# Kernel optimization log

Measured on AMD Instinct MI355X. Metric: run time of the kernel, lower is better.

## Reference

```python
import jax, jax.numpy as jnp
import numpy as np

MASK_VALUE = -10000000.0


def setup_inputs() -> dict:
    key = jax.random.key(0)
    ks = jax.random.split(key, 8)
    U, I, J, C, E = 128, 256, 512, 128, 128
    return {
        "target_items_context": jax.random.normal(ks[0], (U, I, C), jnp.float32),
        "interacted_items_context": jax.random.normal(ks[1], (U, J, C), jnp.float32),
        "user_embeds": jax.random.normal(ks[2], (U, E), jnp.float32),
        "attention_mask": jax.random.randint(ks[3], (U, J), 0, 2) > 0,
        "w_dense": jax.random.normal(ks[4], (2 * C,), jnp.float32) * 0.02,
        "b_dense": jax.random.normal(ks[5], (1,), jnp.float32) * 0.02,
        "W_mlp": jax.random.normal(ks[6], (E + C, C), jnp.float32) * 0.02,
        "b_mlp": jax.random.normal(ks[7], (C,), jnp.float32) * 0.02,
    }


def reference(target_items_context, interacted_items_context, user_embeds,
              attention_mask, w_dense, b_dense, W_mlp, b_mlp):
    C = target_items_context.shape[-1]
    E = user_embeds.shape[-1]
    # additive attention score: tanh([t; k] @ w + b) = tanh(t@w1 + k@w2 + b)
    # (dropout is identity in eval mode)
    s_t = jnp.einsum('uic,c->ui', target_items_context, w_dense[:C])      # (U, I)
    s_k = jnp.einsum('ujc,c->uj', interacted_items_context, w_dense[C:])  # (U, J)
    scores = jnp.tanh(s_t[:, :, None] + s_k[:, None, :] + b_dense[0])     # (U, I, J)
    scores = scores + (~attention_mask)[:, None, :].astype(scores.dtype) * MASK_VALUE
    attn = jax.nn.softmax(scores, axis=-1)                                # (U, I, J)
    # weighted pooling of interacted contexts
    pooled = jnp.einsum('uij,ujc->uic', attn, interacted_items_context)   # (U, I, C)
    # mlp: relu([user; pooled] @ W + b) = relu(user@W[:E] + pooled@W[E:] + b)
    u_part = user_embeds @ W_mlp[:E]                                      # (U, C)
    user_context = jax.nn.relu(u_part[:, None, :] + pooled @ W_mlp[E:] + b_mlp)
    return user_context, attn
```

## Files before the change

### kernel.cpp

```cpp
#include <hip/hip_runtime.h>

#define UU 128
#define II 256
#define JJ 512
#define CC 128
#define EE 128
#define IB2 32
#define NIB2 8
#define JT 64
#define NJT 8
#define VTP 72
#define IBF 16

typedef short bf16x8 __attribute__((ext_vector_type(8)));
typedef float f32x4 __attribute__((ext_vector_type(4)));

union FragU { bf16x8 v; unsigned u[4]; };

__device__ __forceinline__ float fast_tanh(float x) {
    float ex = __expf(2.0f * x);
    return 1.0f - 2.0f / (ex + 1.0f);
}

__device__ __forceinline__ unsigned pack_bf16x2(float lo, float hi) {
    unsigned ul = __float_as_uint(lo), uh = __float_as_uint(hi);
    ul = (ul + 0x7FFFu + ((ul >> 16) & 1u)) >> 16;
    uh = (uh + 0x7FFFu + ((uh >> 16) & 1u)) >> 16;
    return ul | (uh << 16);
}

__device__ __forceinline__ short bf16s(float f) {
    unsigned u = __float_as_uint(f);
    u = (u + 0x7FFFu + ((u >> 16) & 1u)) >> 16;
    return (short)u;
}

__device__ __forceinline__ float wave_reduce_add(float v) {
#pragma unroll
    for (int k = 32; k >= 1; k >>= 1) v += __shfl_xor(v, k, 64);
    return v;
}

#define VT_BLOCKS (UU * NJT)
#define UP_BLOCKS (UU * CC / 256)

__global__ void precompute_kernel(const float* __restrict__ itc,
                                  const float* __restrict__ user,
                                  const float* __restrict__ wd,
                                  const float* __restrict__ Wm,
                                  const float* __restrict__ bm,
                                  float* __restrict__ sk_g,
                                  float* __restrict__ up_g,
                                  short* __restrict__ vtg,
                                  short* __restrict__ wtg) {
    __shared__ float vt_f[JT][CC + 4];
    int b = blockIdx.x;
    int t = threadIdx.x;
    if (b < VT_BLOCKS) {
        int u = b & 127, jt = b >> 7;
        const float* src = itc + ((size_t)u * JJ + jt * JT) * CC;
#pragma unroll
        for (int k = 0; k < 8; ++k) {
            int f = t + 256 * k;
            int row = f >> 5, c4 = (f & 31) * 4;
            f32x4 v = __builtin_nontemporal_load(
                (const f32x4*)&src[(size_t)row * CC + c4]);
            *(f32x4*)&vt_f[row][c4] = v;
        }
        __syncthreads();
        {
            int r = t >> 2, q4 = t & 3;
            float s = 0.f;
#pragma unroll
            for (int cc = 0; cc < 32; cc += 4) {
                float4 a = *(const float4*)&vt_f[r][q4 * 32 + cc];
                float4 w = *(const float4*)&wd[CC + q4 * 32 + cc];
                s += a.x * w.x + a.y * w.y + a.z * w.z + a.w * w.w;
            }
            s += __shfl_xor(s, 1, 64);
            s += __shfl_xor(s, 2, 64);
            if (q4 == 0) sk_g[u * JJ + jt * JT + r] = s;
        }
        {
            int c = t & 127, half = t >> 7;
            unsigned* dst = (unsigned*)(vtg + (size_t)(u * NJT + jt) * 8192) +
                            half * 2048 + c * 16;
#pragma unroll
            for (int m4 = 0; m4 < 4; ++m4) {
                unsigned q[4];
#pragma unroll
                for (int mm = 0; mm < 4; ++mm) {
                    int m = 4 * m4 + mm;
                    q[mm] = pack_bf16x2(vt_f[32 * half + 2 * m][c],
                                        vt_f[32 * half + 2 * m + 1][c]);
                }
                *(uint4*)&dst[4 * m4] = make_uint4(q[0], q[1], q[2], q[3]);
            }
        }
    } else if (b < VT_BLOCKS + UP_BLOCKS) {
        int idx = (b - VT_BLOCKS) * 256 + t;
        int u = idx >> 7, c = idx & 127;
        float acc = bm[c];
#pragma unroll 8
        for (int e = 0; e < EE; ++e) acc += user[u * EE + e] * Wm[e * CC + c];
        up_g[idx] = acc;
    } else {
        int n = t & 127, khalf = t >> 7;
#pragma unroll
        for (int ks2 = 0; ks2 < 2; ++ks2) {
            int ks = khalf * 2 + ks2;
#pragma unroll
            for (int g = 0; g < 4; ++g) {
                unsigned q[4];
#pragma unroll
                for (int pr = 0; pr < 4; ++pr) {
                    float lo = Wm[(size_t)(EE + 32 * ks + 8 * g + 2 * pr) * CC + n];
                    float hi = Wm[(size_t)(EE + 32 * ks + 8 * g + 2 * pr + 1) * CC + n];
                    q[pr] = pack_bf16x2(lo, hi);
                }
                *(uint4*)&wtg[ks * 4096 + n * 32 + 8 * g] =
                    make_uint4(q[0], q[1], q[2], q[3]);
            }
        }
    }
}

__global__ __launch_bounds__(256, 4) void fused_main(
    const float* __restrict__ tgt, const int* __restrict__ mask,
    const float* __restrict__ wd, const float* __restrict__ bd,
    const float* __restrict__ sk_g, const float* __restrict__ up_g,
    const short* __restrict__ vt_g, const short* __restrict__ wt_g,
    float* __restrict__ out_ctx, float* __restrict__ out_attn) {
    __shared__ __align__(16) short ps[16384];
    __shared__ float dinv_lds[IB2];

    int b = blockIdx.x;
    int x = b & 7, q = b >> 3;
    int u = x + 8 * (q >> 3);
    int ib = q & 7;
    int i0 = ib * IB2;
    int t = threadIdx.x;
    int w = t >> 6, l = t & 63, ln = l & 15, g = l >> 4;
    int r2 = t >> 3, seg8 = t & 7;
    int tile = r2 >> 4, rr = r2 & 15;

    float sv;
    {
        const float* trow = tgt + ((size_t)(u * II + i0 + r2)) * CC + seg8 * 16;
        f32x4 t0 = __builtin_nontemporal_load((const f32x4*)&trow[0]);
        f32x4 t1 = __builtin_nontemporal_load((const f32x4*)&trow[4]);
        f32x4 t2 = __builtin_nontemporal_load((const f32x4*)&trow[8]);
        f32x4 t3 = __builtin_nontemporal_load((const f32x4*)&trow[12]);
        float4 w0 = *(const float4*)&wd[seg8 * 16];
        float4 w1 = *(const float4*)&wd[seg8 * 16 + 4];
        float4 w2 = *(const float4*)&wd[seg8 * 16 + 8];
        float4 w3 = *(const float4*)&wd[seg8 * 16 + 12];
        float part = t0[0] * w0.x + t0[1] * w0.y + t0[2] * w0.z + t0[3] * w0.w +
                     t1[0] * w1.x + t1[1] * w1.y + t1[2] * w1.z + t1[3] * w1.w +
                     t2[0] * w2.x + t2[1] * w2.y + t2[2] * w2.z + t2[3] * w2.w +
                     t3[0] * w3.x + t3[1] * w3.y + t3[2] * w3.z + t3[3] * w3.w;
        part += __shfl_xor(part, 1, 64);
        part += __shfl_xor(part, 2, 64);
        part += __shfl_xor(part, 4, 64);
        sv = part + bd[0];
    }

    const float* skb = sk_g + u * JJ;
    const int* mkb = mask + u * JJ;
    char* psrow = (char*)ps + tile * 16384 + rr * 1024;
    float rowsum = 0.f;
#pragma unroll 4
    for (int h = 0; h < 8; ++h) {
        int gcol = seg8 + 8 * h;
        int jb = gcol * 8;
        float4 k0 = *(const float4*)&skb[jb];
        float4 k1 = *(const float4*)&skb[jb + 4];
        int4 m0 = *(const int4*)&mkb[jb];
        int4 m1 = *(const int4*)&mkb[jb + 4];
        float p0 = m0.x ? __expf(fast_tanh(sv + k0.x)) : 0.f;
        float p1 = m0.y ? __expf(fast_tanh(sv + k0.y)) : 0.f;
        float p2 = m0.z ? __expf(fast_tanh(sv + k0.z)) : 0.f;
        float p3 = m0.w ? __expf(fast_tanh(sv + k0.w)) : 0.f;
        float p4 = m1.x ? __expf(fast_tanh(sv + k1.x)) : 0.f;
        float p5 = m1.y ? __expf(fast_tanh(sv + k1.y)) : 0.f;
        float p6 = m1.z ? __expf(fast_tanh(sv + k1.z)) : 0.f;
        float p7 = m1.w ? __expf(fast_tanh(sv + k1.w)) : 0.f;
        rowsum += p0 + p1 + p2 + p3 + p4 + p5 + p6 + p7;
        unsigned q0 = pack_bf16x2(p0, p1);
        unsigned q1 = pack_bf16x2(p2, p3);
        unsigned q2 = pack_bf16x2(p4, p5);
        unsigned q3 = pack_bf16x2(p6, p7);
        int gp = gcol ^ (rr & 7);
        *(uint4*)(psrow + 16 * gp) = make_uint4(q0, q1, q2, q3);
    }
    rowsum += __shfl_xor(rowsum, 1, 64);
    rowsum += __shfl_xor(rowsum, 2, 64);
    rowsum += __shfl_xor(rowsum, 4, 64);
    if (seg8 == 0) dinv_lds[r2] = 1.0f / rowsum;

    const short* b_base =
        vt_g + (size_t)u * (NJT * 8192) + (32 * w + ln) * 32 + 8 * g;
    bf16x8 pb0[4], pb1[4];
#pragma unroll
    for (int s = 0; s < 4; ++s) {
        int off = (s >> 1) * 8192 + (s & 1) * 4096;
        pb0[s] = *(const bf16x8*)&b_base[off];
        pb1[s] = *(const bf16x8*)&b_base[off + 512];
    }

    asm volatile("s_waitcnt lgkmcnt(0)" ::: "memory");
    __builtin_amdgcn_s_barrier();
    asm volatile("" ::: "memory");

    f32x4 a00 = {0.f, 0.f, 0.f, 0.f}, a01 = {0.f, 0.f, 0.f, 0.f};
    f32x4 a10 = {0.f, 0.f, 0.f, 0.f}, a11 = {0.f, 0.f, 0.f, 0.f};
    __builtin_amdgcn_s_setprio(1);
#pragma unroll
    for (int s = 0; s < 16; ++s) {
        int abyte = ln * 1024 + 16 * ((4 * s + g) ^ (ln & 7));
        bf16x8 af0 = *(const bf16x8*)((const char*)ps + abyte);
        bf16x8 af1 = *(const bf16x8*)((const char*)ps + 16384 + abyte);
        a00 = __builtin_amdgcn_mfma_f32_16x16x32_bf16(af0, pb0[s & 3], a00, 0, 0, 0);
        a01 = __builtin_amdgcn_mfma_f32_16x16x32_bf16(af0, pb1[s & 3], a01, 0, 0, 0);
        a10 = __builtin_amdgcn_mfma_f32_16x16x32_bf16(af1, pb0[s & 3], a10, 0, 0, 0);
        a11 = __builtin_amdgcn_mfma_f32_16x16x32_bf16(af1, pb1[s & 3], a11, 0, 0, 0);
        if (s < 12) {
            int off = ((s + 4) >> 1) * 8192 + ((s + 4) & 1) * 4096;
            pb0[s & 3] = *(const bf16x8*)&b_base[off];
            pb1[s & 3] = *(const bf16x8*)&b_base[off + 512];
        }
    }
    __builtin_amdgcn_s_setprio(0);

    const short* wbase = wt_g + (32 * w + ln) * 32 + 8 * g;
    bf16x8 wb0[4], wb1[4];
#pragma unroll
    for (int ks = 0; ks < 4; ++ks) {
        wb0[ks] = *(const bf16x8*)&wbase[ks * 4096];
        wb1[ks] = *(const bf16x8*)&wbase[ks * 4096 + 512];
    }
    int c0 = 32 * w + ln, c1 = c0 + 16;
    float up0v = up_g[u * CC + c0];
    float up1v = up_g[u * CC + c1];

    {
        float* ab = out_attn + ((size_t)(u * II + i0)) * JJ;
#pragma unroll
        for (int k = 0; k < 16; ++k) {
            int f = t + 256 * k;
            int row = f >> 7;
            int j4 = (f & 127) * 4;
            int gcol = j4 >> 3, half = (j4 >> 2) & 1;
            int tl = row >> 4, rw = row & 15;
            uint2 qv = *(const uint2*)((const char*)ps + tl * 16384 + rw * 1024 +
                                       16 * (gcol ^ (rw & 7)) + 8 * half);
            float dv = dinv_lds[row];
            f32x4 v;
            v[0] = __uint_as_float(qv.x << 16) * dv;
            v[1] = __uint_as_float(qv.x & 0xFFFF0000u) * dv;
            v[2] = __uint_as_float(qv.y << 16) * dv;
            v[3] = __uint_as_float(qv.y & 0xFFFF0000u) * dv;
            __builtin_nontemporal_store(v, (f32x4*)&ab[(size_t)row * JJ + j4]);
        }
    }

    asm volatile("s_waitcnt lgkmcnt(0)" ::: "memory");
    __builtin_amdgcn_s_barrier();
    asm volatile("" ::: "memory");

    {
        char* pool = (char*)ps;
#pragma unroll
        for (int ri = 0; ri < 4; ++ri) {
            int row0 = 4 * g + ri, row1 = 16 + row0;
            float dv0 = dinv_lds[row0], dv1 = dinv_lds[row1];
            *(short*)(pool + row0 * 256 + 16 * ((c0 >> 3) ^ (row0 & 7)) +
                      2 * (ln & 7)) = bf16s(a00[ri] * dv0);
            *(short*)(pool + row0 * 256 + 16 * ((c1 >> 3) ^ (row0 & 7)) +
                      2 * (ln & 7)) = bf16s(a01[ri] * dv0);
            *(short*)(pool + row1 * 256 + 16 * ((c0 >> 3) ^ (row1 & 7)) +
                      2 * (ln & 7)) = bf16s(a10[ri] * dv1);
            *(short*)(pool + row1 * 256 + 16 * ((c1 >> 3) ^ (row1 & 7)) +
                      2 * (ln & 7)) = bf16s(a11[ri] * dv1);
        }
    }
    asm volatile("s_waitcnt lgkmcnt(0)" ::: "memory");
    __builtin_amdgcn_s_barrier();
    asm volatile("" ::: "memory");

    f32x4 o00 = {0.f, 0.f, 0.f, 0.f}, o01 = {0.f, 0.f, 0.f, 0.f};
    f32x4 o10 = {0.f, 0.f, 0.f, 0.f}, o11 = {0.f, 0.f, 0.f, 0.f};
#pragma unroll
    for (int ks = 0; ks < 4; ++ks) {
        int pbyte0 = ln * 256 + 16 * ((4 * ks + g) ^ (ln & 7));
        bf16x8 pa0 = *(const bf16x8*)((const char*)ps + pbyte0);
        bf16x8 pa1 = *(const bf16x8*)((const char*)ps + 4096 + pbyte0);
        o00 = __builtin_amdgcn_mfma_f32_16x16x32_bf16(pa0, wb0[ks], o00, 0, 0, 0);
        o01 = __builtin_amdgcn_mfma_f32_16x16x32_bf16(pa0, wb1[ks], o01, 0, 0, 0);
        o10 = __builtin_amdgcn_mfma_f32_16x16x32_bf16(pa1, wb0[ks], o10, 0, 0, 0);
        o11 = __builtin_amdgcn_mfma_f32_16x16x32_bf16(pa1, wb1[ks], o11, 0, 0, 0);
    }
    {
        float* ctx = out_ctx + ((size_t)(u * II + i0)) * CC;
#pragma unroll
        for (int ri = 0; ri < 4; ++ri) {
            int row0 = 4 * g + ri, row1 = 16 + row0;
            __builtin_nontemporal_store(fmaxf(o00[ri] + up0v, 0.f),
                                        &ctx[(size_t)row0 * CC + c0]);
            __builtin_nontemporal_store(fmaxf(o01[ri] + up1v, 0.f),
                                        &ctx[(size_t)row0 * CC + c1]);
            __builtin_nontemporal_store(fmaxf(o10[ri] + up0v, 0.f),
                                        &ctx[(size_t)row1 * CC + c0]);
            __builtin_nontemporal_store(fmaxf(o11[ri] + up1v, 0.f),
                                        &ctx[(size_t)row1 * CC + c1]);
        }
    }
}

__global__ __launch_bounds__(256, 3) void fused_fallback(
    const float* __restrict__ tgt, const float* __restrict__ itc,
    const float* __restrict__ user, const int* __restrict__ mask,
    const float* __restrict__ wd, const float* __restrict__ bd,
    const float* __restrict__ Wm, const float* __restrict__ bm,
    float* __restrict__ out_ctx, float* __restrict__ out_attn) {
    __shared__ __align__(16) short Vt[CC][VTP];
    __shared__ __align__(16) float pool[IBF][CC + 4];
    __shared__ __align__(16) float skv[JJ];
    __shared__ __align__(16) float stv[IBF];
    __shared__ __align__(16) float upv[CC];
    __shared__ __align__(16) float dinv_lds[IBF];
    __shared__ unsigned char mk[JJ];

    int b = blockIdx.x;
    int x = b & 7, q = b >> 3;
    int u = x + 8 * (q >> 4);
    int ib = q & 15;
    int i0 = ib * IBF;
    int t = threadIdx.x;

    mk[t] = (unsigned char)(mask[u * JJ + t] != 0);
    mk[t + 256] = (unsigned char)(mask[u * JJ + t + 256] != 0);

    {
        int lane = t & 63, w4 = t >> 6;
        float2 w2 = *(const float2*)&wd[CC + lane * 2];
        for (int r = w4; r < JJ; r += 4) {
            float2 a = *(const float2*)&itc[((size_t)u * JJ + r) * CC + lane * 2];
            float s = wave_reduce_add(a.x * w2.x + a.y * w2.y);
            if (lane == 0) skv[r] = s;
        }
        float2 w1 = *(const float2*)&wd[lane * 2];
        float bdv = bd[0];
        for (int r = w4; r < IBF; r += 4) {
            float2 a = *(const float2*)&tgt[((size_t)u * II + i0 + r) * CC + lane * 2];
            float s = wave_reduce_add(a.x * w1.x + a.y * w1.y);
            if (lane == 0) stv[r] = s + bdv;
        }
        if (t < CC) {
            float acc = bm[t];
            for (int e = 0; e < EE; ++e) acc += user[u * EE + e] * Wm[e * CC + t];
            upv[t] = acc;
        }
    }
    __syncthreads();

    const int l = t & 63;
    const int w = t >> 6;
    const int ln = l & 15;
    const int g = l >> 4;

    bf16x8 a[16];
    float rowsum = 0.0f;
    {
        float s = stv[ln];
#pragma unroll
        for (int t16 = 0; t16 < 16; ++t16) {
            int j = 32 * t16 + 8 * g;
            float4 k0 = *(const float4*)&skv[j];
            float4 k1 = *(const float4*)&skv[j + 4];
            unsigned m0 = *(const unsigned*)&mk[j];
            unsigned m1 = *(const unsigned*)&mk[j + 4];
            float pf[8];
            pf[0] = (m0 & 0x000000FFu) ? __expf(fast_tanh(s + k0.x)) : 0.0f;
            pf[1] = (m0 & 0x0000FF00u) ? __expf(fast_tanh(s + k0.y)) : 0.0f;
            pf[2] = (m0 & 0x00FF0000u) ? __expf(fast_tanh(s + k0.z)) : 0.0f;
            pf[3] = (m0 & 0xFF000000u) ? __expf(fast_tanh(s + k0.w)) : 0.0f;
            pf[4] = (m1 & 0x000000FFu) ? __expf(fast_tanh(s + k1.x)) : 0.0f;
            pf[5] = (m1 & 0x0000FF00u) ? __expf(fast_tanh(s + k1.y)) : 0.0f;
            pf[6] = (m1 & 0x00FF0000u) ? __expf(fast_tanh(s + k1.z)) : 0.0f;
            pf[7] = (m1 & 0xFF000000u) ? __expf(fast_tanh(s + k1.w)) : 0.0f;
            rowsum += pf[0] + pf[1] + pf[2] + pf[3] + pf[4] + pf[5] + pf[6] + pf[7];
            FragU cu;
            cu.u[0] = pack_bf16x2(pf[0], pf[1]);
            cu.u[1] = pack_bf16x2(pf[2], pf[3]);
            cu.u[2] = pack_bf16x2(pf[4], pf[5]);
            cu.u[3] = pack_bf16x2(pf[6], pf[7]);
            a[t16] = cu.v;
        }
    }
    rowsum += __shfl_xor(rowsum, 16, 64);
    rowsum += __shfl_xor(rowsum, 32, 64);
    float dinv = 1.0f / rowsum;
    if (t < 16) dinv_lds[t] = dinv;

    {
        float* abase = out_attn + ((size_t)(u * II + i0 + ln)) * JJ + 8 * g;
#pragma unroll
        for (int t16 = 0; t16 < 16; ++t16) {
            FragU cu; cu.v = a[t16];
            float f0 = __uint_as_float(cu.u[0] << 16) * dinv;
            float f1 = __uint_as_float(cu.u[0] & 0xFFFF0000u) * dinv;
            float f2 = __uint_as_float(cu.u[1] << 16) * dinv;
            float f3 = __uint_as_float(cu.u[1] & 0xFFFF0000u) * dinv;
            float f4 = __uint_as_float(cu.u[2] << 16) * dinv;
            float f5 = __uint_as_float(cu.u[2] & 0xFFFF0000u) * dinv;
            float f6 = __uint_as_float(cu.u[3] << 16) * dinv;
            float f7 = __uint_as_float(cu.u[3] & 0xFFFF0000u) * dinv;
            *(float4*)&abase[32 * t16] = make_float4(f0, f1, f2, f3);
            *(float4*)&abase[32 * t16 + 4] = make_float4(f4, f5, f6, f7);
        }
    }

    f32x4 acc0 = {0.f, 0.f, 0.f, 0.f};
    f32x4 acc1 = {0.f, 0.f, 0.f, 0.f};
    const float* Vu = itc + (size_t)u * JJ * CC;
    const int cg = t & 31;
    const int jp = t >> 5;
    const int n0 = w * 32;

    for (int jt = 0; jt < 8; ++jt) {
        int j0 = jt * JT;
        __syncthreads();
#pragma unroll
        for (int it = 0; it < 4; ++it) {
            int jl = 2 * (jp + 8 * it);
            const float* r0 = &Vu[(size_t)(j0 + jl) * CC];
            const float* r1 = r0 + CC;
#pragma unroll
            for (int qv = 0; qv < 4; ++qv) {
                int c = cg + 32 * qv;
                *(unsigned*)&Vt[c][jl] = pack_bf16x2(r0[c], r1[c]);
            }
        }
        __syncthreads();
#pragma unroll
        for (int kk = 0; kk < 2; ++kk) {
            bf16x8 b0 = *(const bf16x8*)&Vt[n0 + ln][32 * kk + 8 * g];
            bf16x8 b1 = *(const bf16x8*)&Vt[n0 + 16 + ln][32 * kk + 8 * g];
            acc0 = __builtin_amdgcn_mfma_f32_16x16x32_bf16(a[2 * jt + kk], b0,
                                                           acc0, 0, 0, 0);
            acc1 = __builtin_amdgcn_mfma_f32_16x16x32_bf16(a[2 * jt + kk], b1,
                                                           acc1, 0, 0, 0);
        }
    }

    __syncthreads();
    {
        float4 dv = *(const float4*)&dinv_lds[4 * g];
        float dvr[4] = {dv.x, dv.y, dv.z, dv.w};
#pragma unroll
        for (int r = 0; r < 4; ++r) {
            pool[4 * g + r][n0 + ln] = acc0[r] * dvr[r];
            pool[4 * g + r][n0 + 16 + ln] = acc1[r] * dvr[r];
        }
    }
    __syncthreads();

    {
        int tx = t & 15, ty = t >> 4;
        float o[8];
#pragma unroll
        for (int k = 0; k < 8; ++k) o[k] = 0.f;
#pragma unroll 4
        for (int k = 0; k < CC; ++k) {
            float pk = pool[ty][k];
            float4 w0 = *(const float4*)&Wm[(size_t)(EE + k) * CC + tx * 8];
            float4 w1 = *(const float4*)&Wm[(size_t)(EE + k) * CC + tx * 8 + 4];
            o[0] += pk * w0.x; o[1] += pk * w0.y; o[2] += pk * w0.z; o[3] += pk * w0.w;
            o[4] += pk * w1.x; o[5] += pk * w1.y; o[6] += pk * w1.z; o[7] += pk * w1.w;
        }
        float4 up0 = *(const float4*)&upv[tx * 8];
        float4 up1 = *(const float4*)&upv[tx * 8 + 4];
        float4 r0, r1;
        r0.x = fmaxf(o[0] + up0.x, 0.f); r0.y = fmaxf(o[1] + up0.y, 0.f);
        r0.z = fmaxf(o[2] + up0.z, 0.f); r0.w = fmaxf(o[3] + up0.w, 0.f);
        r1.x = fmaxf(o[4] + up1.x, 0.f); r1.y = fmaxf(o[5] + up1.y, 0.f);
        r1.z = fmaxf(o[6] + up1.z, 0.f); r1.w = fmaxf(o[7] + up1.w, 0.f);
        float* ctx = out_ctx + ((size_t)(u * II + i0 + ty)) * CC + tx * 8;
        *(float4*)&ctx[0] = r0;
        *(float4*)&ctx[4] = r1;
    }
}

extern "C" void kernel_launch(void* const* d_in, const int* in_sizes, int n_in,
                              void* d_out, int out_size, void* d_ws,
                              size_t ws_size, hipStream_t stream) {
    const float* tgt  = (const float*)d_in[0];
    const float* itc  = (const float*)d_in[1];
    const float* user = (const float*)d_in[2];
    const int*   mask = (const int*)d_in[3];
    const float* wd   = (const float*)d_in[4];
    const float* bd   = (const float*)d_in[5];
    const float* Wm   = (const float*)d_in[6];
    const float* bm   = (const float*)d_in[7];
    float* out_ctx  = (float*)d_out;
    float* out_attn = out_ctx + (size_t)UU * II * CC;

    size_t scalars = (size_t)(UU * JJ + UU * CC) * sizeof(float);
    size_t vt_bytes = (size_t)UU * NJT * 8192 * sizeof(short);
    size_t wt_bytes = (size_t)16384 * sizeof(short);
    size_t need = scalars + vt_bytes + wt_bytes;
    if (ws_size >= need) {
        float* sk_g = (float*)d_ws;
        float* up_g = sk_g + UU * JJ;
        short* vt_g = (short*)((char*)d_ws + scalars);
        short* wt_g = vt_g + (size_t)UU * NJT * 8192;
        int gridA = VT_BLOCKS + UP_BLOCKS + 1;
        precompute_kernel<<<gridA, 256, 0, stream>>>(itc, user, wd, Wm, bm,
                                                     sk_g, up_g, vt_g, wt_g);
        fused_main<<<UU * NIB2, 256, 0, stream>>>(tgt, mask, wd, bd, sk_g, up_g,
                                                  vt_g, wt_g, out_ctx, out_attn);
    } else {
        fused_fallback<<<UU * (II / IBF), 256, 0, stream>>>(
            tgt, itc, user, mask, wd, bd, Wm, bm, out_ctx, out_attn);
    }
}
```

Baseline: 50.50 us.

## Specialize warps: two waves do the P@V MFMA while two stream the attention output

Work between the four waves is now split by role. Waves 0-1 each compute 64 output columns of the attention-weighted pooling with MFMA, double-buffering their V fragments. Waves 2-3 write the normalized attention matrix to global memory, which lets the global store traffic overlap with the matrix-core work. The cost is that MFMA throughput is concentrated in half the waves and register pressure rises in those waves (eight accumulators).

```diff
diff --git a/kernel.cpp b/kernel.cpp
--- a/kernel.cpp
+++ b/kernel.cpp
@@ -198,69 +198,85 @@
     rowsum += __shfl_xor(rowsum, 4, 64);
     if (seg8 == 0) dinv_lds[r2] = 1.0f / rowsum;
 
-    const short* b_base =
-        vt_g + (size_t)u * (NJT * 8192) + (32 * w + ln) * 32 + 8 * g;
-    bf16x8 pb0[4], pb1[4];
-#pragma unroll
-    for (int s = 0; s < 4; ++s) {
-        int off = (s >> 1) * 8192 + (s & 1) * 4096;
-        pb0[s] = *(const bf16x8*)&b_base[off];
-        pb1[s] = *(const bf16x8*)&b_base[off + 512];
-    }
-
     asm volatile("s_waitcnt lgkmcnt(0)" ::: "memory");
     __builtin_amdgcn_s_barrier();
     asm volatile("" ::: "memory");
 
-    f32x4 a00 = {0.f, 0.f, 0.f, 0.f}, a01 = {0.f, 0.f, 0.f, 0.f};
-    f32x4 a10 = {0.f, 0.f, 0.f, 0.f}, a11 = {0.f, 0.f, 0.f, 0.f};
-    __builtin_amdgcn_s_setprio(1);
-#pragma unroll
-    for (int s = 0; s < 16; ++s) {
-        int abyte = ln * 1024 + 16 * ((4 * s + g) ^ (ln & 7));
-        bf16x8 af0 = *(const bf16x8*)((const char*)ps + abyte);
-        bf16x8 af1 = *(const bf16x8*)((const char*)ps + 16384 + abyte);
-        a00 = __builtin_amdgcn_mfma_f32_16x16x32_bf16(af0, pb0[s & 3], a00, 0, 0, 0);
-        a01 = __builtin_amdgcn_mfma_f32_16x16x32_bf16(af0, pb1[s & 3], a01, 0, 0, 0);
-        a10 = __builtin_amdgcn_mfma_f32_16x16x32_bf16(af1, pb0[s & 3], a10, 0, 0, 0);
-        a11 = __builtin_amdgcn_mfma_f32_16x16x32_bf16(af1, pb1[s & 3], a11, 0, 0, 0);
-        if (s < 12) {
-            int off = ((s + 4) >> 1) * 8192 + ((s + 4) & 1) * 4096;
-            pb0[s & 3] = *(const bf16x8*)&b_base[off];
-            pb1[s & 3] = *(const bf16x8*)&b_base[off + 512];
-        }
-    }
-    __builtin_amdgcn_s_setprio(0);
-
-    const short* wbase = wt_g + (32 * w + ln) * 32 + 8 * g;
+    f32x4 acc0[4], acc1[4];
     bf16x8 wb0[4], wb1[4];
-#pragma unroll
-    for (int ks = 0; ks < 4; ++ks) {
-        wb0[ks] = *(const bf16x8*)&wbase[ks * 4096];
-        wb1[ks] = *(const bf16x8*)&wbase[ks * 4096 + 512];
-    }
+    float up0v = 0.f, up1v = 0.f;
     int c0 = 32 * w + ln, c1 = c0 + 16;
-    float up0v = up_g[u * CC + c0];
-    float up1v = up_g[u * CC + c1];
-
-    {
-        float* ab = out_attn + ((size_t)(u * II + i0)) * JJ;
-#pragma unroll
-        for (int k = 0; k < 16; ++k) {
-            int f = t + 256 * k;
-            int row = f >> 7;
-            int j4 = (f & 127) * 4;
-            int gcol = j4 >> 3, half = (j4 >> 2) & 1;
-            int tl = row >> 4, rw = row & 15;
+
+    if (w < 2) {
+        const short* bb[4];
+#pragma unroll
+        for (int n = 0; n < 4; ++n)
+            bb[n] = vt_g + (size_t)u * (NJT * 8192) +
+                    (16 * (4 * w + n) + ln) * 32 + 8 * g;
+        bf16x8 pbA[4], pbB[4];
+#pragma unroll
+        for (int n = 0; n < 4; ++n) pbA[n] = *(const bf16x8*)&bb[n][0];
+        {
+            f32x4 z = {0.f, 0.f, 0.f, 0.f};
+#pragma unroll
+            for (int n = 0; n < 4; ++n) { acc0[n] = z; acc1[n] = z; }
+        }
+        __builtin_amdgcn_s_setprio(1);
+#pragma unroll
+        for (int s = 0; s < 16; ++s) {
+            if (s < 15) {
+                int off = ((s + 1) >> 1) * 8192 + ((s + 1) & 1) * 4096;
+#pragma unroll
+                for (int n = 0; n < 4; ++n) {
+                    if (s & 1) pbA[n] = *(const bf16x8*)&bb[n][off];
+                    else       pbB[n] = *(const bf16x8*)&bb[n][off];
+                }
+            }
+            int abyte = ln * 1024 + 16 * ((4 * s + g) ^ (ln & 7));
+            bf16x8 af0 = *(const bf16x8*)((const char*)ps + abyte);
+            bf16x8 af1 = *(const bf16x8*)((const char*)ps + 16384 + abyte);
+#pragma unroll
+            for (int n = 0; n < 4; ++n) {
+                bf16x8 bf = (s & 1) ? pbB[n] : pbA[n];
+                acc0[n] = __builtin_amdgcn_mfma_f32_16x16x32_bf16(af0, bf,
+                                                                  acc0[n], 0, 0, 0);
+                acc1[n] = __builtin_amdgcn_mfma_f32_16x16x32_bf16(af1, bf,
+                                                                  acc1[n], 0, 0, 0);
+            }
+        }
+        __builtin_amdgcn_s_setprio(0);
+        const short* wbase = wt_g + (32 * w + ln) * 32 + 8 * g;
+#pragma unroll
+        for (int ks = 0; ks < 4; ++ks) {
+            wb0[ks] = *(const bf16x8*)&wbase[ks * 4096];
+            wb1[ks] = *(const bf16x8*)&wbase[ks * 4096 + 512];
+        }
+        up0v = up_g[u * CC + c0];
+        up1v = up_g[u * CC + c1];
+    } else {
+        const short* wbase = wt_g + (32 * w + ln) * 32 + 8 * g;
+#pragma unroll
+        for (int ks = 0; ks < 4; ++ks) {
+            wb0[ks] = *(const bf16x8*)&wbase[ks * 4096];
+            wb1[ks] = *(const bf16x8*)&wbase[ks * 4096 + 512];
+        }
+        up0v = up_g[u * CC + c0];
+        up1v = up_g[u * CC + c1];
+
+        int tt = t & 127;
+        float* ab = out_attn + ((size_t)(u * II + i0)) * JJ + tt * 4;
+#pragma unroll
+        for (int k = 0; k < 32; ++k) {
+            int tl = k >> 4, rw = k & 15;
             uint2 qv = *(const uint2*)((const char*)ps + tl * 16384 + rw * 1024 +
-                                       16 * (gcol ^ (rw & 7)) + 8 * half);
-            float dv = dinv_lds[row];
+                                       16 * ((tt >> 1) ^ (rw & 7)) + 8 * (tt & 1));
+            float dv = dinv_lds[k];
             f32x4 v;
             v[0] = __uint_as_float(qv.x << 16) * dv;
             v[1] = __uint_as_float(qv.x & 0xFFFF0000u) * dv;
             v[2] = __uint_as_float(qv.y << 16) * dv;
             v[3] = __uint_as_float(qv.y & 0xFFFF0000u) * dv;
-            __builtin_nontemporal_store(v, (f32x4*)&ab[(size_t)row * JJ + j4]);
+            __builtin_nontemporal_store(v, (f32x4*)&ab[(size_t)k * JJ]);
         }
     }
 
@@ -268,20 +284,20 @@
     __builtin_amdgcn_s_barrier();
     asm volatile("" ::: "memory");
 
-    {
+    if (w < 2) {
         char* pool = (char*)ps;
 #pragma unroll
-        for (int ri = 0; ri < 4; ++ri) {
-            int row0 = 4 * g + ri, row1 = 16 + row0;
-            float dv0 = dinv_lds[row0], dv1 = dinv_lds[row1];
-            *(short*)(pool + row0 * 256 + 16 * ((c0 >> 3) ^ (row0 & 7)) +
-                      2 * (ln & 7)) = bf16s(a00[ri] * dv0);
-            *(short*)(pool + row0 * 256 + 16 * ((c1 >> 3) ^ (row0 & 7)) +
-                      2 * (ln & 7)) = bf16s(a01[ri] * dv0);
-            *(short*)(pool + row1 * 256 + 16 * ((c0 >> 3) ^ (row1 & 7)) +
-                      2 * (ln & 7)) = bf16s(a10[ri] * dv1);
-            *(short*)(pool + row1 * 256 + 16 * ((c1 >> 3) ^ (row1 & 7)) +
-                      2 * (ln & 7)) = bf16s(a11[ri] * dv1);
+        for (int n = 0; n < 4; ++n) {
+            int c = 16 * (4 * w + n) + ln;
+            int gcol = c >> 3;
+#pragma unroll
+            for (int ri = 0; ri < 4; ++ri) {
+                int row0 = 4 * g + ri, row1 = 16 + row0;
+                *(short*)(pool + row0 * 256 + 16 * (gcol ^ (row0 & 7)) +
+                          2 * (ln & 7)) = bf16s(acc0[n][ri] * dinv_lds[row0]);
+                *(short*)(pool + row1 * 256 + 16 * (gcol ^ (row1 & 7)) +
+                          2 * (ln & 7)) = bf16s(acc1[n][ri] * dinv_lds[row1]);
+            }
         }
     }
     asm volatile("s_waitcnt lgkmcnt(0)" ::: "memory");
```

Result: slower. 51.80 us (+2.6%).
